# Performance work log

Measured on AMD Instinct MI355X. Metric: run time of the kernel, lower is better.

## Reference

```python
import jax, jax.numpy as jnp
import numpy as np

DIM = 4096          # power of two -> no padding branch
LAYERS = 12         # log2(DIM)
BATCH = 8192


def setup_inputs() -> dict:
    key = jax.random.key(0)
    kx, ka = jax.random.split(key)
    x = jax.random.normal(kx, (BATCH, DIM), dtype=jnp.float32)
    # original init: uniform(-0.05, 0.05) per layer of DIM//2 angles
    angles = jax.random.uniform(ka, (LAYERS, DIM // 2), dtype=jnp.float32,
                                minval=-0.05, maxval=0.05)
    return {"x": x, "angles": angles}


def reference(x, angles):
    """Butterfly O(d log d) rotation. x:(B,d), angles:(L, d//2).

    Layer l pairs elements (j, j+stride), stride=2**l. The torch code's
    angle index for pair offset i in block starting at `start` is
    start//2 + i, which equals reshaping theta to (num_blocks, stride).
    """
    B, d = x.shape
    out = x
    for l in range(LAYERS):
        stride = 1 << l
        nb = d // (2 * stride)              # blocks per layer
        theta = angles[l].reshape(nb, stride)
        c = jnp.cos(theta)                  # (nb, stride)
        s = jnp.sin(theta)
        o = out.reshape(B, nb, 2, stride)
        xl = o[:, :, 0, :]                  # (B, nb, stride)
        xr = o[:, :, 1, :]
        new_l = c * xl + s * xr
        new_r = -s * xl + c * xr
        out = jnp.stack([new_l, new_r], axis=2).reshape(B, d)
    return out
```

## Files before the change

kernel.cpp:

```cpp
#include <hip/hip_runtime.h>
#include <hip/hip_fp16.h>


#define DIM    4096
#define LAYERS 12
#define BATCH  8192
#define NANG   2048
#define BLOCK  512

typedef unsigned int u32;
typedef float v2f __attribute__((ext_vector_type(2)));

#define BAR() do {                                             \
    asm volatile("s_waitcnt lgkmcnt(0)" ::: "memory");         \
    __builtin_amdgcn_sched_barrier(0);                         \
    __builtin_amdgcn_s_barrier();                              \
} while (0)

__device__ __forceinline__ int swzQ(int Q) {
    return Q ^ ((Q >> 3) & 7) ^ ((Q >> 6) & 7);
}
__device__ __forceinline__ int uslot(int e) {
    return 2 * swzQ(e >> 1) + (e & 1);
}
__device__ __forceinline__ constexpr int inner_idx(int m, int jj) {
    return ((m >> (jj + 1)) << jj) + (m & ((1 << jj) - 1));
}

__device__ __forceinline__ void rot2(v2f& xl, v2f& xr, float c, float s) {
    v2f nl = c * xl + s * xr;
    v2f nr = c * xr - s * xl;
    xl = nl; xr = nr;
}

__global__ void __launch_bounds__(256) cs_kernel(const float* __restrict__ angles,
                                                 u32* __restrict__ TH, int n) {
    int i = blockIdx.x * blockDim.x + threadIdx.x;
    if (i >= n) return;
    float a = angles[i];
    float c = cosf(a), s = sinf(a);
    int l = i >> 11, aa = i & 2047;
    int region, jj, t, ii;
    if (l < 3)      { region = 0; jj = l;     t = aa >> 2;  ii = aa & 3; }
    else if (l < 6) { region = 1; jj = l - 3; int B = aa >> 5, r = aa & 31;
                      ii = r >> 3; t = 8 * B + (r & 7); }
    else if (l < 9) { region = 2; jj = l - 6; int S = aa >> 8, r = aa & 255;
                      ii = r >> 6; t = 64 * S + (r & 63); }
    else            { region = 3; jj = l - 9; ii = aa >> 9; t = aa & 511; }
    int a_idx = jj * 4 + ii;
    int flat = ((region * 3 + (a_idx >> 2)) * 512 + t) * 4 + (a_idx & 3);
    u32 lo = (u32)__half_as_ushort(__float2half(1.0f - c));
    u32 hi = (u32)__half_as_ushort(__float2half(s));
    TH[flat] = lo | (hi << 16);
}

#define UNPACK12(Ua, Ub, Uc, ca, sa) do {                                  \
    const u32 _u[12] = {Ua.x, Ua.y, Ua.z, Ua.w, Ub.x, Ub.y, Ub.z, Ub.w,    \
                        Uc.x, Uc.y, Uc.z, Uc.w};                           \
    _Pragma("unroll")                                                      \
    for (int a = 0; a < 12; ++a) {                                         \
        __half2 h2 = *reinterpret_cast<const __half2*>(&_u[a]);            \
        float2 f = __half22float2(h2);                                     \
        ca[a] = 1.0f - f.x;                                                \
        sa[a] = f.y;                                                       \
    }                                                                      \
} while (0)

#define PHASE_ROTS(ca, sa, w)                                              \
    _Pragma("unroll")                                                      \
    for (int jj = 0; jj < 3; ++jj) {                                       \
        const int st = 1 << jj;                                            \
        _Pragma("unroll")                                                  \
        for (int m = 0; m < 8; ++m) {                                      \
            if (!(m & st)) {                                               \
                const int a = jj * 4 + inner_idx(m, jj);                   \
                rot2(w[m], w[m + st], ca[a], sa[a]);                       \
            }                                                              \
        }                                                                  \
    }

__global__ void __launch_bounds__(BLOCK, 6)
butterfly_kernel(const float* __restrict__ x, const uint4* __restrict__ TH4,
                 float* __restrict__ out) {
    __shared__ v2f buf[DIM];
    const int t = threadIdx.x;
    const long row0 = (long)blockIdx.x * 2;

    v2f w[8];
    float ca[12], sa[12];

    {
        uint4 A0 = TH4[0 * 512 + t], A1 = TH4[1 * 512 + t], A2 = TH4[2 * 512 + t];
        const float* p0 = x + row0 * DIM + 8 * t;
        const float* p1 = p0 + DIM;
        float4 a = *(const float4*)(p0),     b = *(const float4*)(p0 + 4);
        float4 c = *(const float4*)(p1),     d = *(const float4*)(p1 + 4);
        uint4 B0 = TH4[3 * 512 + t], B1 = TH4[4 * 512 + t], B2 = TH4[5 * 512 + t];

        w[0] = v2f{a.x, c.x}; w[1] = v2f{a.y, c.y};
        w[2] = v2f{a.z, c.z}; w[3] = v2f{a.w, c.w};
        w[4] = v2f{b.x, d.x}; w[5] = v2f{b.y, d.y};
        w[6] = v2f{b.z, d.z}; w[7] = v2f{b.w, d.w};
        UNPACK12(A0, A1, A2, ca, sa);
        PHASE_ROTS(ca, sa, w)
        #pragma unroll
        for (int q = 0; q < 4; ++q) {
            *(float4*)(&buf[2 * swzQ(4 * t + q)]) =
                make_float4(w[2*q].x, w[2*q].y, w[2*q+1].x, w[2*q+1].y);
        }
        BAR();

        uint4 C0 = TH4[6 * 512 + t], C1 = TH4[7 * 512 + t], C2 = TH4[8 * 512 + t];
        {
            const int eb = 64 * (t >> 3) + (t & 7);
            int ps[8];
            #pragma unroll
            for (int m = 0; m < 8; ++m) {
                ps[m] = uslot(eb + 8 * m);
                w[m] = buf[ps[m]];
            }
            UNPACK12(B0, B1, B2, ca, sa);
            PHASE_ROTS(ca, sa, w)
            #pragma unroll
            for (int m = 0; m < 8; ++m) buf[ps[m]] = w[m];
        }
        BAR();

        uint4 D0 = TH4[9 * 512 + t], D1 = TH4[10 * 512 + t], D2 = TH4[11 * 512 + t];
        {
            const int eb = 512 * (t >> 6) + (t & 63);
            int ps[8];
            #pragma unroll
            for (int m = 0; m < 8; ++m) {
                ps[m] = uslot(eb + 64 * m);
                w[m] = buf[ps[m]];
            }
            UNPACK12(C0, C1, C2, ca, sa);
            PHASE_ROTS(ca, sa, w)
            #pragma unroll
            for (int m = 0; m < 8; ++m) buf[ps[m]] = w[m];
        }
        BAR();

        {
            #pragma unroll
            for (int m = 0; m < 8; ++m) w[m] = buf[uslot(t + 512 * m)];
            UNPACK12(D0, D1, D2, ca, sa);
            PHASE_ROTS(ca, sa, w)
            float* o0 = out + row0 * DIM + t;
            float* o1 = o0 + DIM;
            #pragma unroll
            for (int m = 0; m < 8; ++m) {
                __builtin_nontemporal_store(w[m].x, o0 + (m << 9));
                __builtin_nontemporal_store(w[m].y, o1 + (m << 9));
            }
        }
    }
}

extern "C" void kernel_launch(void* const* d_in, const int* in_sizes, int n_in,
                              void* d_out, int out_size, void* d_ws, size_t ws_size,
                              hipStream_t stream) {
    (void)in_sizes; (void)n_in; (void)out_size; (void)ws_size;
    const float* x      = (const float*)d_in[0];
    const float* angles = (const float*)d_in[1];
    float* out = (float*)d_out;

    const int n = LAYERS * NANG;
    cs_kernel<<<(n + 255) / 256, 256, 0, stream>>>(angles, (u32*)d_ws, n);
    butterfly_kernel<<<BATCH / 2, BLOCK, 0, stream>>>(x, (const uint4*)d_ws, out);
}
```

Measured before the change: 53.40 us.

## Replace middle LDS exchange phases with cross-lane swizzle and bpermute butterflies

Layers 3 through 8 now run as in-register butterflies across wavefront lanes, using ds_swizzle for strides 1-16 lanes and ds_bpermute for stride 32, instead of two LDS write/read phases with barriers. The angle table is re-laid out per layer so each lane loads its own cos/sin values, with partner lanes sharing the same entry. This removes two block barriers and two rounds of LDS traffic. In exchange each layer issues twice the cross-lane permute ops and loads more angle-table entries per thread.

```diff
diff --git a/kernel.cpp b/kernel.cpp
--- a/kernel.cpp
+++ b/kernel.cpp
@@ -39,19 +39,25 @@
     if (i >= n) return;
     float a = angles[i];
     float c = cosf(a), s = sinf(a);
-    int l = i >> 11, aa = i & 2047;
-    int region, jj, t, ii;
-    if (l < 3)      { region = 0; jj = l;     t = aa >> 2;  ii = aa & 3; }
-    else if (l < 6) { region = 1; jj = l - 3; int B = aa >> 5, r = aa & 31;
-                      ii = r >> 3; t = 8 * B + (r & 7); }
-    else if (l < 9) { region = 2; jj = l - 6; int S = aa >> 8, r = aa & 255;
-                      ii = r >> 6; t = 64 * S + (r & 63); }
-    else            { region = 3; jj = l - 9; ii = aa >> 9; t = aa & 511; }
-    int a_idx = jj * 4 + ii;
-    int flat = ((region * 3 + (a_idx >> 2)) * 512 + t) * 4 + (a_idx & 3);
     u32 lo = (u32)__half_as_ushort(__float2half(1.0f - c));
     u32 hi = (u32)__half_as_ushort(__float2half(s));
-    TH[flat] = lo | (hi << 16);
+    u32 packed = lo | (hi << 16);
+    int l = i >> 11, aa = i & 2047;
+    if (l < 3) {
+        int t = aa >> 2, ii = aa & 3;
+        TH[((l * 512) + t) * 4 + ii] = packed;
+    } else if (l < 9) {
+        int hi_ = aa >> l, lo_ = aa & ((1 << l) - 1);
+        int e_left = (hi_ << (l + 1)) + lo_;
+        int k = e_left & 7;
+        int tL = e_left >> 3;
+        int group = 3 + (l - 3) * 2 + (k >> 2);
+        TH[((group * 512) + tL) * 4 + (k & 3)] = packed;
+    } else {
+        int ii = aa >> 9, t = aa & 511;
+        int group = 15 + (l - 9);
+        TH[((group * 512) + t) * 4 + ii] = packed;
+    }
 }
 
 #define UNPACK12(Ua, Ub, Uc, ca, sa) do {                                  \
@@ -79,81 +85,120 @@
         }                                                                  \
     }
 
+template<int IMM>
+__device__ __forceinline__ v2f swz2(v2f v) {
+    int x = __builtin_amdgcn_ds_swizzle(__float_as_int(v.x), IMM);
+    int y = __builtin_amdgcn_ds_swizzle(__float_as_int(v.y), IMM);
+    return v2f{__int_as_float(x), __int_as_float(y)};
+}
+__device__ __forceinline__ v2f bperm2(v2f v, int bidx) {
+    int x = __builtin_amdgcn_ds_bpermute(bidx, __float_as_int(v.x));
+    int y = __builtin_amdgcn_ds_bpermute(bidx, __float_as_int(v.y));
+    return v2f{__int_as_float(x), __int_as_float(y)};
+}
+
+template<int LBIT, int IMM>
+__device__ __forceinline__ void shfl_layer(v2f* w, const uint4& Ua,
+                                           const uint4& Ub, int lane) {
+    float cc[8], ss[8];
+    {
+        const u32 _u[8] = {Ua.x, Ua.y, Ua.z, Ua.w, Ub.x, Ub.y, Ub.z, Ub.w};
+        #pragma unroll
+        for (int a = 0; a < 8; ++a) {
+            __half2 h2 = *reinterpret_cast<const __half2*>(&_u[a]);
+            float2 f = __half22float2(h2);
+            cc[a] = 1.0f - f.x;
+            ss[a] = f.y;
+        }
+    }
+    const u32 smask = (lane & LBIT) ? 0x80000000u : 0u;
+    #pragma unroll
+    for (int m = 0; m < 8; ++m) {
+        v2f other = swz2<IMM>(w[m]);
+        float se = __int_as_float(__float_as_int(ss[m]) ^ smask);
+        w[m] = cc[m] * w[m] + se * other;
+    }
+}
+
 __global__ void __launch_bounds__(BLOCK, 6)
 butterfly_kernel(const float* __restrict__ x, const uint4* __restrict__ TH4,
                  float* __restrict__ out) {
     __shared__ v2f buf[DIM];
     const int t = threadIdx.x;
+    const int lane = t & 63;
     const long row0 = (long)blockIdx.x * 2;
 
     v2f w[8];
     float ca[12], sa[12];
 
-    {
-        uint4 A0 = TH4[0 * 512 + t], A1 = TH4[1 * 512 + t], A2 = TH4[2 * 512 + t];
+    uint4 A0 = TH4[0 * 512 + t], A1 = TH4[1 * 512 + t], A2 = TH4[2 * 512 + t];
+    {
         const float* p0 = x + row0 * DIM + 8 * t;
         const float* p1 = p0 + DIM;
-        float4 a = *(const float4*)(p0),     b = *(const float4*)(p0 + 4);
-        float4 c = *(const float4*)(p1),     d = *(const float4*)(p1 + 4);
-        uint4 B0 = TH4[3 * 512 + t], B1 = TH4[4 * 512 + t], B2 = TH4[5 * 512 + t];
-
+        float4 a = *(const float4*)(p0),  b = *(const float4*)(p0 + 4);
+        float4 c = *(const float4*)(p1),  d = *(const float4*)(p1 + 4);
         w[0] = v2f{a.x, c.x}; w[1] = v2f{a.y, c.y};
         w[2] = v2f{a.z, c.z}; w[3] = v2f{a.w, c.w};
         w[4] = v2f{b.x, d.x}; w[5] = v2f{b.y, d.y};
         w[6] = v2f{b.z, d.z}; w[7] = v2f{b.w, d.w};
-        UNPACK12(A0, A1, A2, ca, sa);
-        PHASE_ROTS(ca, sa, w)
-        #pragma unroll
-        for (int q = 0; q < 4; ++q) {
-            *(float4*)(&buf[2 * swzQ(4 * t + q)]) =
-                make_float4(w[2*q].x, w[2*q].y, w[2*q+1].x, w[2*q+1].y);
-        }
-        BAR();
-
-        uint4 C0 = TH4[6 * 512 + t], C1 = TH4[7 * 512 + t], C2 = TH4[8 * 512 + t];
-        {
-            const int eb = 64 * (t >> 3) + (t & 7);
-            int ps[8];
-            #pragma unroll
-            for (int m = 0; m < 8; ++m) {
-                ps[m] = uslot(eb + 8 * m);
-                w[m] = buf[ps[m]];
-            }
-            UNPACK12(B0, B1, B2, ca, sa);
-            PHASE_ROTS(ca, sa, w)
-            #pragma unroll
-            for (int m = 0; m < 8; ++m) buf[ps[m]] = w[m];
-        }
-        BAR();
-
-        uint4 D0 = TH4[9 * 512 + t], D1 = TH4[10 * 512 + t], D2 = TH4[11 * 512 + t];
-        {
-            const int eb = 512 * (t >> 6) + (t & 63);
-            int ps[8];
-            #pragma unroll
-            for (int m = 0; m < 8; ++m) {
-                ps[m] = uslot(eb + 64 * m);
-                w[m] = buf[ps[m]];
-            }
-            UNPACK12(C0, C1, C2, ca, sa);
-            PHASE_ROTS(ca, sa, w)
-            #pragma unroll
-            for (int m = 0; m < 8; ++m) buf[ps[m]] = w[m];
-        }
-        BAR();
-
-        {
-            #pragma unroll
-            for (int m = 0; m < 8; ++m) w[m] = buf[uslot(t + 512 * m)];
-            UNPACK12(D0, D1, D2, ca, sa);
-            PHASE_ROTS(ca, sa, w)
-            float* o0 = out + row0 * DIM + t;
-            float* o1 = o0 + DIM;
-            #pragma unroll
-            for (int m = 0; m < 8; ++m) {
-                __builtin_nontemporal_store(w[m].x, o0 + (m << 9));
-                __builtin_nontemporal_store(w[m].y, o1 + (m << 9));
-            }
+    }
+    uint4 B0 = TH4[3 * 512 + (t & ~1)],  B1 = TH4[4 * 512 + (t & ~1)];
+
+    UNPACK12(A0, A1, A2, ca, sa);
+    PHASE_ROTS(ca, sa, w)
+
+    uint4 C0 = TH4[5 * 512 + (t & ~2)],  C1 = TH4[6 * 512 + (t & ~2)];
+    shfl_layer<1, 0x041F>(w, B0, B1, lane);
+    B0 = TH4[7 * 512 + (t & ~4)];  B1 = TH4[8 * 512 + (t & ~4)];
+    shfl_layer<2, 0x081F>(w, C0, C1, lane);
+    C0 = TH4[9 * 512 + (t & ~8)];  C1 = TH4[10 * 512 + (t & ~8)];
+    shfl_layer<4, 0x101F>(w, B0, B1, lane);
+    B0 = TH4[11 * 512 + (t & ~16)]; B1 = TH4[12 * 512 + (t & ~16)];
+    shfl_layer<8, 0x201F>(w, C0, C1, lane);
+    C0 = TH4[13 * 512 + (t & ~32)]; C1 = TH4[14 * 512 + (t & ~32)];
+    shfl_layer<16, 0x401F>(w, B0, B1, lane);
+
+    uint4 D0 = TH4[15 * 512 + t], D1 = TH4[16 * 512 + t], D2 = TH4[17 * 512 + t];
+
+    {
+        float cc[8], ss[8];
+        const u32 _u[8] = {C0.x, C0.y, C0.z, C0.w, C1.x, C1.y, C1.z, C1.w};
+        #pragma unroll
+        for (int a = 0; a < 8; ++a) {
+            __half2 h2 = *reinterpret_cast<const __half2*>(&_u[a]);
+            float2 f = __half22float2(h2);
+            cc[a] = 1.0f - f.x;
+            ss[a] = f.y;
+        }
+        const u32 smask = (lane & 32) ? 0x80000000u : 0u;
+        const int bidx = (lane ^ 32) << 2;
+        #pragma unroll
+        for (int m = 0; m < 8; ++m) {
+            v2f other = bperm2(w[m], bidx);
+            float se = __int_as_float(__float_as_int(ss[m]) ^ smask);
+            w[m] = cc[m] * w[m] + se * other;
+        }
+    }
+
+    #pragma unroll
+    for (int q = 0; q < 4; ++q) {
+        *(float4*)(&buf[2 * swzQ(4 * t + q)]) =
+            make_float4(w[2*q].x, w[2*q].y, w[2*q+1].x, w[2*q+1].y);
+    }
+    BAR();
+    #pragma unroll
+    for (int m = 0; m < 8; ++m) w[m] = buf[uslot(t + 512 * m)];
+
+    UNPACK12(D0, D1, D2, ca, sa);
+    PHASE_ROTS(ca, sa, w)
+
+    {
+        float* o0 = out + row0 * DIM + t;
+        float* o1 = o0 + DIM;
+        #pragma unroll
+        for (int m = 0; m < 8; ++m) {
+            __builtin_nontemporal_store(w[m].x, o0 + (m << 9));
+            __builtin_nontemporal_store(w[m].y, o1 + (m << 9));
         }
     }
 }
```

Result: slower. 57.53 us (+7.7%).
